# Optimization experiments

Measured on AMD Instinct MI355X. Metric: run time of the kernel, lower is better.

Reference implementation:

```python
import jax, jax.numpy as jnp
import numpy as np

CLAMP_MIN, CLAMP_MAX = 1e-7, 10.0


def _hyper_layer(H, edge_nodes, W, b, power):
    """One HyperTensorGraphConvolution forward.

    H:          [N, d] node signals
    edge_nodes: [E, k] int node indices per hyperedge (k-1 < num_sample, so
                the sampling branch of the original code never triggers and the
                aggregation is the full power-mean over the k-1 neighbors)
    """
    H = jnp.clip(H, CLAMP_MIN, CLAMP_MAX)          # torch.clamp_(H, ...)
    inv_p = 1.0 / power
    Hp = H ** power                                 # [N, d]
    gathered = Hp[edge_nodes]                       # [E, k, d]
    edge_sum = gathered.sum(axis=1, keepdims=True)  # [E, 1, d]
    k = edge_nodes.shape[1]
    # power-mean of the other (k-1) nodes in the hyperedge, per incidence
    contrib = ((edge_sum - gathered) / (k - 1)) ** inv_p   # [E, k, d]
    # new_signal = H.clone(); scatter-add contributions per (edge, node)
    d = H.shape[1]
    new_signal = H.at[edge_nodes.reshape(-1)].add(contrib.reshape(-1, d))
    # row-normalize (rowsum^-1, inf -> 0)
    rowsum = new_signal.sum(axis=1, keepdims=True)
    r_inv = jnp.where(rowsum != 0, 1.0 / rowsum, 0.0)
    AH = new_signal * r_inv
    return AH @ W + b


def setup_inputs() -> dict:
    key = jax.random.key(0)
    k_x, k_e, k_w1, k_b1, k_w2, k_b2 = jax.random.split(key, 6)
    N, d, E, k, c = 100000, 128, 25000, 32, 40
    x = jax.random.uniform(k_x, (N, d), dtype=jnp.float32)
    edge_nodes = jax.random.randint(k_e, (E, k), 0, N, dtype=jnp.int64)
    std1 = 1.0 / np.sqrt(16.0)
    W1 = jax.random.uniform(k_w1, (d, 16), jnp.float32, -std1, std1)
    b1 = jax.random.uniform(k_b1, (16,), jnp.float32, -std1, std1)
    std2 = 1.0 / np.sqrt(float(c))
    W2 = jax.random.uniform(k_w2, (16, c), jnp.float32, -std2, std2)
    b2 = jax.random.uniform(k_b2, (c,), jnp.float32, -std2, std2)
    return {"x": x, "edge_nodes": edge_nodes, "W1": W1, "b1": b1,
            "W2": W2, "b2": b2, "power": 2}


def reference(x, edge_nodes, W1, b1, W2, b2, power):
    H = jax.nn.relu(_hyper_layer(x, edge_nodes, W1, b1, float(power)))
    # dropout is identity at inference
    out = _hyper_layer(H, edge_nodes, W2, b2, float(power))
    return out
```

## Files before the change

### kernel.cpp

```cpp
#include <hip/hip_runtime.h>
#include <hip/hip_fp16.h>
#include <math.h>

#define CAP 64
#define D1 128
#define D2 16
#define C_OUT 40
#define K_EDGE 32
#define CLAMP_LO 1e-7f
#define CLAMP_HI 10.0f
#define SQRT_INV31 0.1796053020267749f

typedef unsigned short ushort_t;
typedef _Float16 h2v __attribute__((ext_vector_type(2)));

__global__ __launch_bounds__(256) void k_setup(const float* __restrict__ x,
                                               __half2* __restrict__ Hp,
                                               const float* __restrict__ W1,
                                               float* __restrict__ W1t,
                                               __half2* __restrict__ S,
                                               float* __restrict__ S2,
                                               int* __restrict__ deg,
                                               int n4, int N, int E) {
    int i = blockIdx.x * 256 + threadIdx.x;
    if (i < n4) {
        float4 v = ((const float4*)x)[i];
        v.x = fminf(fmaxf(v.x, CLAMP_LO), CLAMP_HI);
        v.y = fminf(fmaxf(v.y, CLAMP_LO), CLAMP_HI);
        v.z = fminf(fmaxf(v.z, CLAMP_LO), CLAMP_HI);
        v.w = fminf(fmaxf(v.w, CLAMP_LO), CLAMP_HI);
        __half2 h0 = __floats2half2_rn(v.x * v.x, v.y * v.y);
        __half2 h1 = __floats2half2_rn(v.z * v.z, v.w * v.w);
        uint2 st;
        __builtin_memcpy(&st.x, &h0, 4);
        __builtin_memcpy(&st.y, &h1, 4);
        ((uint2*)Hp)[i] = st;
    }
    if (i < N) deg[i] = 0;
    if (i < D1 * D2) W1t[(i & 15) * D1 + (i >> 4)] = W1[i];
    if (i < 64) S[(size_t)E * 64 + i] = __floats2half2_rn(0.0f, 0.0f);
    if (i < D2) S2[(size_t)E * D2 + i] = 0.0f;
}

__global__ __launch_bounds__(256) void k_edge_sum(const __half2* __restrict__ Hp,
                                                  const int* __restrict__ idx,
                                                  __half2* __restrict__ S,
                                                  int* __restrict__ deg,
                                                  ushort_t* __restrict__ lst, int E) {
    int w = threadIdx.x >> 6;
    int lane = threadIdx.x & 63;
    int eA = blockIdx.x * 8 + w * 2;
    int nid = idx[eA * K_EDGE + lane];
    float a0 = 0.0f, a1 = 0.0f, b0 = 0.0f, b1 = 0.0f;
#pragma unroll
    for (int j = 0; j < K_EDGE; j++) {
        int nA = __builtin_amdgcn_readlane(nid, j);
        int nB = __builtin_amdgcn_readlane(nid, 32 + j);
        __half2 hA = Hp[(size_t)nA * 64 + lane];
        __half2 hB = Hp[(size_t)nB * 64 + lane];
        a0 += __low2float(hA); a1 += __high2float(hA);
        b0 += __low2float(hB); b1 += __high2float(hB);
    }
    int e_of = eA + (lane >> 5);
    int pos = atomicAdd(&deg[nid], 1);
    if (pos < CAP) lst[(size_t)nid * CAP + pos] = (ushort_t)e_of;

    S[(size_t)eA * 64 + lane]       = __floats2half2_rn(a0, a1);
    S[(size_t)(eA + 1) * 64 + lane] = __floats2half2_rn(b0, b1);
}

#define SQ4(p, s, base, hp)                                                   \
    {                                                                         \
        h2v d0_ = __builtin_elementwise_max((s)[(base) + 0] - (hp), zv);      \
        h2v d1_ = __builtin_elementwise_max((s)[(base) + 1] - (hp), zv);      \
        h2v d2_ = __builtin_elementwise_max((s)[(base) + 2] - (hp), zv);      \
        h2v d3_ = __builtin_elementwise_max((s)[(base) + 3] - (hp), zv);      \
        p = __builtin_elementwise_sqrt(d0_) + __builtin_elementwise_sqrt(d1_) \
          + __builtin_elementwise_sqrt(d2_) + __builtin_elementwise_sqrt(d3_);\
    }

__global__ __launch_bounds__(256) void k_node1(const __half2* __restrict__ Hp,
                                               const __half2* __restrict__ S,
                                               const int* __restrict__ deg,
                                               const ushort_t* __restrict__ lst,
                                               const float* __restrict__ W1t,
                                               const float* __restrict__ b1,
                                               float* __restrict__ Hp2, int N, int E) {
    int w = threadIdx.x >> 6;
    int lane = threadIdx.x & 63;
    int quad = blockIdx.x * 4 + w;
    int n0 = quad * 4;
    int c = lane & 15, j = lane >> 4;
    int sl = lane & 15, g = lane >> 4;

    int4 d4 = ((const int4*)deg)[quad];
    int dgA = min(d4.x, CAP), dgB = min(d4.y, CAP);
    int dgC = min(d4.z, CAP), dgD = min(d4.w, CAP);

    ushort_t idu = lst[(n0 + g) * CAP + sl];
    int dsel = (g == 0) ? dgA : (g == 1) ? dgB : (g == 2) ? dgC : dgD;
    int e_sel = (sl < dsel) ? (int)idu : E;

    __half2 hphA = Hp[(size_t)(n0 + 0) * 64 + lane];
    __half2 hphB = Hp[(size_t)(n0 + 1) * 64 + lane];
    __half2 hphC = Hp[(size_t)(n0 + 2) * 64 + lane];
    __half2 hphD = Hp[(size_t)(n0 + 3) * 64 + lane];
    h2v hpA, hpB, hpC, hpD;
    __builtin_memcpy(&hpA, &hphA, 4);
    __builtin_memcpy(&hpB, &hphB, 4);
    __builtin_memcpy(&hpC, &hphC, 4);
    __builtin_memcpy(&hpD, &hphD, 4);
    const h2v zv = (h2v)(_Float16)0.0f;

    int dmAB = max(dgA, dgB);
    int dmCD = max(dgC, dgD);
    int dmax = max(dmAB, dmCD);

    float aA0 = 0.0f, aA1 = 0.0f, aB0 = 0.0f, aB1 = 0.0f;
    float aC0 = 0.0f, aC1 = 0.0f, aD0 = 0.0f, aD1 = 0.0f;

    h2v sA[12], sB[12], sC[12], sD[12];
#pragma unroll
    for (int t = 0; t < 12; t++) {
        int eA = __builtin_amdgcn_readlane(e_sel, t);
        int eB = __builtin_amdgcn_readlane(e_sel, 16 + t);
        int eC = __builtin_amdgcn_readlane(e_sel, 32 + t);
        int eD = __builtin_amdgcn_readlane(e_sel, 48 + t);
        __half2 hv;
        hv = S[(size_t)eA * 64 + lane]; __builtin_memcpy(&sA[t], &hv, 4);
        hv = S[(size_t)eB * 64 + lane]; __builtin_memcpy(&sB[t], &hv, 4);
        hv = S[(size_t)eC * 64 + lane]; __builtin_memcpy(&sC[t], &hv, 4);
        hv = S[(size_t)eD * 64 + lane]; __builtin_memcpy(&sD[t], &hv, 4);
    }

    {
        h2v pA, pB, pC, pD;
        SQ4(pA, sA, 0, hpA);  SQ4(pB, sB, 0, hpB);
        SQ4(pC, sC, 0, hpC);  SQ4(pD, sD, 0, hpD);
        h2v qA, qB, qC, qD;
        SQ4(qA, sA, 4, hpA);  SQ4(qB, sB, 4, hpB);
        SQ4(qC, sC, 4, hpC);  SQ4(qD, sD, 4, hpD);
        aA0 += (float)pA[0] + (float)qA[0];  aA1 += (float)pA[1] + (float)qA[1];
        aB0 += (float)pB[0] + (float)qB[0];  aB1 += (float)pB[1] + (float)qB[1];
        aC0 += (float)pC[0] + (float)qC[0];  aC1 += (float)pC[1] + (float)qC[1];
        aD0 += (float)pD[0] + (float)qD[0];  aD1 += (float)pD[1] + (float)qD[1];
    }

    if (dmAB > 8) {
        h2v pA, pB;
        SQ4(pA, sA, 8, hpA);  SQ4(pB, sB, 8, hpB);
        aA0 += (float)pA[0];  aA1 += (float)pA[1];
        aB0 += (float)pB[0];  aB1 += (float)pB[1];
        if (dmAB > 12) {
            h2v uA[4], uB[4];
#pragma unroll
            for (int t = 0; t < 4; t++) {
                int eA = __builtin_amdgcn_readlane(e_sel, 12 + t);
                int eB = __builtin_amdgcn_readlane(e_sel, 28 + t);
                __half2 hv;
                hv = S[(size_t)eA * 64 + lane]; __builtin_memcpy(&uA[t], &hv, 4);
                hv = S[(size_t)eB * 64 + lane]; __builtin_memcpy(&uB[t], &hv, 4);
            }
            h2v vA, vB;
            SQ4(vA, uA, 0, hpA);  SQ4(vB, uB, 0, hpB);
            aA0 += (float)vA[0];  aA1 += (float)vA[1];
            aB0 += (float)vB[0];  aB1 += (float)vB[1];
        }
    }

    if (dmCD > 8) {
        h2v pC, pD;
        SQ4(pC, sC, 8, hpC);  SQ4(pD, sD, 8, hpD);
        aC0 += (float)pC[0];  aC1 += (float)pC[1];
        aD0 += (float)pD[0];  aD1 += (float)pD[1];
        if (dmCD > 12) {
            h2v uC[4], uD[4];
#pragma unroll
            for (int t = 0; t < 4; t++) {
                int eC = __builtin_amdgcn_readlane(e_sel, 44 + t);
                int eD = __builtin_amdgcn_readlane(e_sel, 60 + t);
                __half2 hv;
                hv = S[(size_t)eC * 64 + lane]; __builtin_memcpy(&uC[t], &hv, 4);
                hv = S[(size_t)eD * 64 + lane]; __builtin_memcpy(&uD[t], &hv, 4);
            }
            h2v vC, vD;
            SQ4(vC, uC, 0, hpC);  SQ4(vD, uD, 0, hpD);
            aC0 += (float)vC[0];  aC1 += (float)vC[1];
            aD0 += (float)vD[0];  aD1 += (float)vD[1];
        }
    }

    if (dmax > 16) {
        float hA0 = (float)hpA[0], hA1 = (float)hpA[1];
        float hB0 = (float)hpB[0], hB1 = (float)hpB[1];
        float hC0 = (float)hpC[0], hC1 = (float)hpC[1];
        float hD0 = (float)hpD[0], hD1 = (float)hpD[1];
        for (int t = 16; t < dgA; t++) {
            int e = lst[(n0 + 0) * CAP + t];
            __half2 sh = S[(size_t)e * 64 + lane];
            aA0 += __builtin_amdgcn_sqrtf(fmaxf(__low2float(sh)  - hA0, 0.0f));
            aA1 += __builtin_amdgcn_sqrtf(fmaxf(__high2float(sh) - hA1, 0.0f));
        }
        for (int t = 16; t < dgB; t++) {
            int e = lst[(n0 + 1) * CAP + t];
            __half2 sh = S[(size_t)e * 64 + lane];
            aB0 += __builtin_amdgcn_sqrtf(fmaxf(__low2float(sh)  - hB0, 0.0f));
            aB1 += __builtin_amdgcn_sqrtf(fmaxf(__high2float(sh) - hB1, 0.0f));
        }
        for (int t = 16; t < dgC; t++) {
            int e = lst[(n0 + 2) * CAP + t];
            __half2 sh = S[(size_t)e * 64 + lane];
            aC0 += __builtin_amdgcn_sqrtf(fmaxf(__low2float(sh)  - hC0, 0.0f));
            aC1 += __builtin_amdgcn_sqrtf(fmaxf(__high2float(sh) - hC1, 0.0f));
        }
        for (int t = 16; t < dgD; t++) {
            int e = lst[(n0 + 3) * CAP + t];
            __half2 sh = S[(size_t)e * 64 + lane];
            aD0 += __builtin_amdgcn_sqrtf(fmaxf(__low2float(sh)  - hD0, 0.0f));
            aD1 += __builtin_amdgcn_sqrtf(fmaxf(__high2float(sh) - hD1, 0.0f));
        }
    }

    float nsA0 = __builtin_amdgcn_sqrtf((float)hpA[0]) + aA0 * SQRT_INV31;
    float nsA1 = __builtin_amdgcn_sqrtf((float)hpA[1]) + aA1 * SQRT_INV31;
    float nsB0 = __builtin_amdgcn_sqrtf((float)hpB[0]) + aB0 * SQRT_INV31;
    float nsB1 = __builtin_amdgcn_sqrtf((float)hpB[1]) + aB1 * SQRT_INV31;
    float nsC0 = __builtin_amdgcn_sqrtf((float)hpC[0]) + aC0 * SQRT_INV31;
    float nsC1 = __builtin_amdgcn_sqrtf((float)hpC[1]) + aC1 * SQRT_INV31;
    float nsD0 = __builtin_amdgcn_sqrtf((float)hpD[0]) + aD0 * SQRT_INV31;
    float nsD1 = __builtin_amdgcn_sqrtf((float)hpD[1]) + aD1 * SQRT_INV31;

    __shared__ float AHs[4][4][D1];
    AHs[w][0][2 * lane] = nsA0;  AHs[w][0][2 * lane + 1] = nsA1;
    AHs[w][1][2 * lane] = nsB0;  AHs[w][1][2 * lane + 1] = nsB1;
    AHs[w][2][2 * lane] = nsC0;  AHs[w][2][2 * lane + 1] = nsC1;
    AHs[w][3][2 * lane] = nsD0;  AHs[w][3][2 * lane + 1] = nsD1;

    float vA = nsA0 + nsA1, vB = nsB0 + nsB1;
    float vC = nsC0 + nsC1, vD = nsD0 + nsD1;
#pragma unroll
    for (int m = 1; m < 64; m <<= 1) {
        vA += __shfl_xor(vA, m, 64);
        vB += __shfl_xor(vB, m, 64);
        vC += __shfl_xor(vC, m, 64);
        vD += __shfl_xor(vD, m, 64);
    }
    float rA = __builtin_amdgcn_rcpf(vA);
    float rB = __builtin_amdgcn_rcpf(vB);
    float rC = __builtin_amdgcn_rcpf(vC);
    float rD = __builtin_amdgcn_rcpf(vD);

    __threadfence_block();

    const float4* aAp = (const float4*)(&AHs[w][0][j * 32]);
    const float4* aBp = (const float4*)(&AHs[w][1][j * 32]);
    const float4* aCp = (const float4*)(&AHs[w][2][j * 32]);
    const float4* aDp = (const float4*)(&AHs[w][3][j * 32]);
    const float4* w1p = (const float4*)(W1t + c * D1 + j * 32);
    float pA = 0.0f, pB = 0.0f, pC = 0.0f, pD = 0.0f;
#pragma unroll
    for (int tt = 0; tt < 8; tt++) {
        float4 wv = w1p[tt];
        float4 xA = aAp[tt];
        float4 xB = aBp[tt];
        float4 xC = aCp[tt];
        float4 xD = aDp[tt];
        pA += xA.x * wv.x + xA.y * wv.y + xA.z * wv.z + xA.w * wv.w;
        pB += xB.x * wv.x + xB.y * wv.y + xB.z * wv.z + xB.w * wv.w;
        pC += xC.x * wv.x + xC.y * wv.y + xC.z * wv.z + xC.w * wv.w;
        pD += xD.x * wv.x + xD.y * wv.y + xD.z * wv.z + xD.w * wv.w;
    }
    pA += __shfl_xor(pA, 16, 64);  pA += __shfl_xor(pA, 32, 64);
    pB += __shfl_xor(pB, 16, 64);  pB += __shfl_xor(pB, 32, 64);
    pC += __shfl_xor(pC, 16, 64);  pC += __shfl_xor(pC, 32, 64);
    pD += __shfl_xor(pD, 16, 64);  pD += __shfl_xor(pD, 32, 64);

    float bb = b1[c];
    float oA = fminf(fmaxf(bb + pA * rA, CLAMP_LO), CLAMP_HI);
    float oB = fminf(fmaxf(bb + pB * rB, CLAMP_LO), CLAMP_HI);
    float oC = fminf(fmaxf(bb + pC * rC, CLAMP_LO), CLAMP_HI);
    float oD = fminf(fmaxf(bb + pD * rD, CLAMP_LO), CLAMP_HI);
    float qA = oA * oA, qB = oB * oB, qC = oC * oC, qD = oD * oD;
    float val = (g == 0) ? qA : (g == 1) ? qB : (g == 2) ? qC : qD;
    Hp2[(size_t)quad * 64 + lane] = val;
}

__global__ __launch_bounds__(256) void k_edge_sum2(const float* __restrict__ Hp2,
                                                   const int* __restrict__ idx,
                                                   float* __restrict__ S2, int E) {
    int e = blockIdx.x * 16 + (threadIdx.x >> 4);
    int col = threadIdx.x & 15;
    if (e >= E) return;
    float acc = 0.0f;
#pragma unroll
    for (int j = 0; j < K_EDGE; j++) {
        int n = idx[e * K_EDGE + j];
        acc += Hp2[(size_t)n * D2 + col];
    }
    S2[(size_t)e * D2 + col] = acc;
}

__global__ __launch_bounds__(256) void k_node2(const float* __restrict__ Hp2,
                                               const float* __restrict__ S2,
                                               const int* __restrict__ deg,
                                               const ushort_t* __restrict__ lst,
                                               const float* __restrict__ W2,
                                               const float* __restrict__ b2,
                                               float* __restrict__ out, int N, int E) {
    int w = threadIdx.x >> 6;
    int lane = threadIdx.x & 63;
    int quad = blockIdx.x * 4 + w;
    int n0 = quad * 4;
    int col = lane & 15;
    int g = lane >> 4;
    int nn = n0 + g;

    int4 d4 = ((const int4*)deg)[quad];
    int dgA = min(d4.x, CAP), dgB = min(d4.y, CAP);
    int dgC = min(d4.z, CAP), dgD = min(d4.w, CAP);
    int dsel = (g == 0) ? dgA : (g == 1) ? dgB : (g == 2) ? dgC : dgD;

    ushort_t idu = lst[(size_t)nn * CAP + col];
    int e_sel = (col < dsel) ? (int)idu : E;

    float hp = Hp2[(size_t)n0 * D2 + lane];
    int dmax = max(max(dgA, dgB), max(dgC, dgD));

    int ev[12];
#pragma unroll
    for (int t = 0; t < 12; t++) ev[t] = __shfl(e_sel, g * 16 + t, 64);
    float sv[12];
#pragma unroll
    for (int t = 0; t < 12; t++) sv[t] = S2[(size_t)ev[t] * D2 + col];

    float acc = 0.0f;
#pragma unroll
    for (int t = 0; t < 8; t++)
        acc += __builtin_amdgcn_sqrtf(fmaxf(sv[t] - hp, 0.0f));
    if (dmax > 8) {
#pragma unroll
        for (int t = 8; t < 12; t++)
            acc += __builtin_amdgcn_sqrtf(fmaxf(sv[t] - hp, 0.0f));
        if (dmax > 12) {
#pragma unroll
            for (int t = 12; t < 16; t++) {
                int e = __shfl(e_sel, g * 16 + t, 64);
                float s = S2[(size_t)e * D2 + col];
                acc += __builtin_amdgcn_sqrtf(fmaxf(s - hp, 0.0f));
            }
        }
    }
    if (dmax > 16) {
        for (int t = 16; t < dsel; t++) {
            int e = lst[(size_t)nn * CAP + t];
            float s = S2[(size_t)e * D2 + col];
            acc += __builtin_amdgcn_sqrtf(fmaxf(s - hp, 0.0f));
        }
    }
    float ns = __builtin_amdgcn_sqrtf(hp) + acc * SQRT_INV31;

    float v = ns;
#pragma unroll
    for (int m = 1; m < 16; m <<= 1) v += __shfl_xor(v, m, 64);
    float r = __builtin_amdgcn_rcpf(v);

    __shared__ float AHs[4][4][D2];
    AHs[w][g][col] = ns * r;
    __threadfence_block();

    if (lane < C_OUT) {
        float o0 = b2[lane], o1 = o0, o2 = o0, o3 = o0;
#pragma unroll
        for (int i = 0; i < D2; i++) {
            float wv = W2[i * C_OUT + lane];
            o0 += AHs[w][0][i] * wv;
            o1 += AHs[w][1][i] * wv;
            o2 += AHs[w][2][i] * wv;
            o3 += AHs[w][3][i] * wv;
        }
        out[(size_t)(n0 + 0) * C_OUT + lane] = o0;
        out[(size_t)(n0 + 1) * C_OUT + lane] = o1;
        out[(size_t)(n0 + 2) * C_OUT + lane] = o2;
        out[(size_t)(n0 + 3) * C_OUT + lane] = o3;
    }
}

extern "C" void kernel_launch(void* const* d_in, const int* in_sizes, int n_in,
                              void* d_out, int out_size, void* d_ws, size_t ws_size,
                              hipStream_t stream) {
    const float* x   = (const float*)d_in[0];
    const int*   idx = (const int*)d_in[1];
    const float* W1  = (const float*)d_in[2];
    const float* b1  = (const float*)d_in[3];
    const float* W2  = (const float*)d_in[4];
    const float* b2  = (const float*)d_in[5];
    float* out = (float*)d_out;

    int N = in_sizes[0] / D1;
    int E = in_sizes[1] / K_EDGE;

    __half2* Hp = (__half2*)d_ws;
    __half2* S  = Hp + (size_t)N * 64;
    float* Hp2  = (float*)(S + (size_t)(E + 1) * 64);
    float* S2   = Hp2 + (size_t)N * D2;
    float* W1t  = S2 + (size_t)(E + 1) * D2;
    int*   deg  = (int*)(W1t + D1 * D2);
    ushort_t* lst = (ushort_t*)(deg + N);

    int n4 = N * D1 / 4;

    k_setup<<<(n4 + 255) / 256, 256, 0, stream>>>(x, Hp, W1, W1t, S, S2, deg,
                                                  n4, N, E);
    k_edge_sum<<<E / 8, 256, 0, stream>>>(Hp, idx, S, deg, lst, E);
    k_node1<<<N / 16, 256, 0, stream>>>(Hp, S, deg, lst, W1t, b1, Hp2, N, E);
    k_edge_sum2<<<(E + 15) / 16, 256, 0, stream>>>(Hp2, idx, S2, E);
    k_node2<<<N / 16, 256, 0, stream>>>(Hp2, S2, deg, lst, W2, b2, out, N, E);
}
```

Measured before the change: 213.3 us.

## Split edge-sum gather into column quarters and pack incidence lists via atomicOr

```diff
diff --git a/kernel.cpp b/kernel.cpp
--- a/kernel.cpp
+++ b/kernel.cpp
@@ -21,6 +21,7 @@
                                                __half2* __restrict__ S,
                                                float* __restrict__ S2,
                                                int* __restrict__ deg,
+                                               uint2* __restrict__ lstz,
                                                int n4, int N, int E) {
     int i = blockIdx.x * 256 + threadIdx.x;
     if (i < n4) {
@@ -36,6 +37,7 @@
         __builtin_memcpy(&st.y, &h1, 4);
         ((uint2*)Hp)[i] = st;
     }
+    if (i < N * 16) lstz[i] = make_uint2(0u, 0u);
     if (i < N) deg[i] = 0;
     if (i < D1 * D2) W1t[(i & 15) * D1 + (i >> 4)] = W1[i];
     if (i < 64) S[(size_t)E * 64 + i] = __floats2half2_rn(0.0f, 0.0f);
@@ -46,27 +48,55 @@
                                                   const int* __restrict__ idx,
                                                   __half2* __restrict__ S,
                                                   int* __restrict__ deg,
-                                                  ushort_t* __restrict__ lst, int E) {
+                                                  unsigned int* __restrict__ lstw,
+                                                  int E) {
     int w = threadIdx.x >> 6;
     int lane = threadIdx.x & 63;
-    int eA = blockIdx.x * 8 + w * 2;
-    int nid = idx[eA * K_EDGE + lane];
+    int q = blockIdx.x & 3;
+    int g = blockIdx.x >> 2;
+    int eA = g * 16 + w * 4;
+    if (eA >= E) return;
+    int col = lane & 15;
+    int ed = lane >> 4;
+    int qoff = q * 16;
+
+    int nid0 = idx[eA * K_EDGE + lane];
+    int nid1 = idx[(eA + 2) * K_EDGE + lane];
+
     float a0 = 0.0f, a1 = 0.0f, b0 = 0.0f, b1 = 0.0f;
+    float c0 = 0.0f, c1 = 0.0f, d0 = 0.0f, d1 = 0.0f;
 #pragma unroll
     for (int j = 0; j < K_EDGE; j++) {
-        int nA = __builtin_amdgcn_readlane(nid, j);
-        int nB = __builtin_amdgcn_readlane(nid, 32 + j);
-        __half2 hA = Hp[(size_t)nA * 64 + lane];
-        __half2 hB = Hp[(size_t)nB * 64 + lane];
+        int nA = __builtin_amdgcn_readlane(nid0, j);
+        int nB = __builtin_amdgcn_readlane(nid0, 32 + j);
+        int nC = __builtin_amdgcn_readlane(nid1, j);
+        int nD = __builtin_amdgcn_readlane(nid1, 32 + j);
+        __half2 hA = Hp[(size_t)nA * 64 + qoff + col];
+        __half2 hB = Hp[(size_t)nB * 64 + qoff + col];
+        __half2 hC = Hp[(size_t)nC * 64 + qoff + col];
+        __half2 hD = Hp[(size_t)nD * 64 + qoff + col];
         a0 += __low2float(hA); a1 += __high2float(hA);
         b0 += __low2float(hB); b1 += __high2float(hB);
-    }
-    int e_of = eA + (lane >> 5);
-    int pos = atomicAdd(&deg[nid], 1);
-    if (pos < CAP) lst[(size_t)nid * CAP + pos] = (ushort_t)e_of;
-
-    S[(size_t)eA * 64 + lane]       = __floats2half2_rn(a0, a1);
-    S[(size_t)(eA + 1) * 64 + lane] = __floats2half2_rn(b0, b1);
+        c0 += __low2float(hC); c1 += __high2float(hC);
+        d0 += __low2float(hD); d1 += __high2float(hD);
+    }
+
+    if (w == q) {
+        int e0 = eA + (lane >> 5);
+        int pos0 = atomicAdd(&deg[nid0], 1);
+        if (pos0 < CAP)
+            atomicOr(&lstw[nid0 * (CAP / 2) + (pos0 >> 1)],
+                     (unsigned int)(ushort_t)e0 << (16 * (pos0 & 1)));
+        int e1 = eA + 2 + (lane >> 5);
+        int pos1 = atomicAdd(&deg[nid1], 1);
+        if (pos1 < CAP)
+            atomicOr(&lstw[nid1 * (CAP / 2) + (pos1 >> 1)],
+                     (unsigned int)(ushort_t)e1 << (16 * (pos1 & 1)));
+    }
+
+    float s0 = (ed == 0) ? a0 : (ed == 1) ? b0 : (ed == 2) ? c0 : d0;
+    float s1 = (ed == 0) ? a1 : (ed == 1) ? b1 : (ed == 2) ? c1 : d1;
+    S[(size_t)(eA + ed) * 64 + qoff + col] = __floats2half2_rn(s0, s1);
 }
 
 #define SQ4(p, s, base, hp)                                                   \
@@ -410,8 +440,10 @@
     int n4 = N * D1 / 4;
 
     k_setup<<<(n4 + 255) / 256, 256, 0, stream>>>(x, Hp, W1, W1t, S, S2, deg,
-                                                  n4, N, E);
-    k_edge_sum<<<E / 8, 256, 0, stream>>>(Hp, idx, S, deg, lst, E);
+                                                  (uint2*)lst, n4, N, E);
+    int g4 = (E + 15) / 16;
+    k_edge_sum<<<4 * g4, 256, 0, stream>>>(Hp, idx, S, deg,
+                                           (unsigned int*)lst, E);
     k_node1<<<N / 16, 256, 0, stream>>>(Hp, S, deg, lst, W1t, b1, Hp2, N, E);
     k_edge_sum2<<<(E + 15) / 16, 256, 0, stream>>>(Hp2, idx, S2, E);
     k_node2<<<N / 16, 256, 0, stream>>>(Hp2, S2, deg, lst, W2, b2, out, N, E);
```

Measured after the change: 241.9 us. 13.4% more time.
